# Optimization experiments

Hardware: AMD Instinct MI355X
Metric: run time of the kernel (lower is better)

## Reference

```python
import jax, jax.numpy as jnp
import numpy as np

N_NODES = 1048576
N_GRAPHS = 4096
NODES_PER_GRAPH = N_NODES // N_GRAPHS
N_EDGES = 8388608
F_IN = 16
HID = 32


def _glorot(k, shp):
    return jax.random.normal(k, shp, jnp.float32) * np.float32(np.sqrt(2.0 / (shp[-2] + shp[-1])))


def setup_inputs() -> dict:
    key = jax.random.key(0)
    ks = jax.random.split(key, 8)
    d = F_IN + HID  # DCRNN gate convs act on cat([X, H])
    return {
        "x": jax.random.normal(ks[0], (N_NODES, F_IN), jnp.float32),
        "edge_index": jax.random.randint(ks[1], (2, N_EDGES), 0, N_NODES),
        "edge_weight": jax.random.uniform(ks[2], (N_EDGES,), jnp.float32),
        "batch": jnp.repeat(jnp.arange(N_GRAPHS), NODES_PER_GRAPH),
        "W_z": _glorot(ks[3], (2, 1, d, HID)),
        "b_z": jnp.zeros((HID,), jnp.float32),
        "W_r": _glorot(ks[4], (2, 1, d, HID)),
        "b_r": jnp.zeros((HID,), jnp.float32),
        "W_h": _glorot(ks[5], (2, 1, d, HID)),
        "b_h": jnp.zeros((HID,), jnp.float32),
        "W_lin": _glorot(ks[6], (HID, 1)),
        "b_lin": jnp.zeros((1,), jnp.float32),
    }


def _dconv_k1(X, W, b):
    # torch_geometric_temporal DConv with K=1: the diffusion loop never runs,
    # so H = X @ W[0,0] + X @ W[1,0] + b (edge_index/edge_weight unused).
    return X @ (W[0, 0] + W[1, 0]) + b


def reference(x, edge_index, edge_weight, batch, W_z, b_z, W_r, b_r, W_h, b_h, W_lin, b_lin):
    del edge_index, edge_weight  # mathematically unused when K=1
    h0 = jnp.zeros((x.shape[0], HID), x.dtype)  # DCRNN hidden state default
    xh = jnp.concatenate([x, h0], axis=1)
    Z = jax.nn.sigmoid(_dconv_k1(xh, W_z, b_z))
    R = jax.nn.sigmoid(_dconv_k1(xh, W_r, b_r))
    xhr = jnp.concatenate([x, h0 * R], axis=1)
    H_tilde = jnp.tanh(_dconv_k1(xhr, W_h, b_h))
    H = Z * h0 + (1.0 - Z) * H_tilde  # (N, 32)
    h = jax.nn.relu(H)
    h = h @ W_lin + b_lin  # (N, 1)
    # global_mean_pool over per-node graph ids
    sums = jax.ops.segment_sum(h, batch, num_segments=N_GRAPHS)
    cnts = jax.ops.segment_sum(jnp.ones((h.shape[0], 1), h.dtype), batch, num_segments=N_GRAPHS)
    return sums / jnp.maximum(cnts, 1.0)  # (N_GRAPHS, 1)
```

## Files before the change

kernel.cpp:

```cpp
#include <hip/hip_runtime.h>

#define N_GRAPHS  4096
#define NPG       256
#define F_IN      16
#define HID       32
#define LOG2E     1.4426950408889634f

#define WS_FLOATS 609

typedef _Float16 half8  __attribute__((ext_vector_type(8)));
typedef float    f32x16 __attribute__((ext_vector_type(16)));

#if __has_builtin(__builtin_amdgcn_exp2f)
#define EXP2(x) __builtin_amdgcn_exp2f(x)
#else
#define EXP2(x) exp2f(x)
#endif

union FragU { uint4 u; half8 h; };

__device__ __forceinline__ uint4 make_frag32(int f, int l,
    const float* __restrict__ Wz, const float* __restrict__ Wh)
{
    const int col = l & 31, p = l >> 5;
    const float s = (f == 0) ? LOG2E : 2.0f * LOG2E;
    const float* W = (f == 0) ? Wz : Wh;
    FragU u;
#pragma unroll
    for (int j = 0; j < 8; ++j) {
        const int k = p * 8 + j;
        u.h[j] = (_Float16)((W[k * 32 + col] + W[1536 + k * 32 + col]) * s);
    }
    return u.u;
}

__global__ __launch_bounds__(256) void prep_kernel(
    const float* __restrict__ Wz, const float* __restrict__ bz,
    const float* __restrict__ Wh, const float* __restrict__ bh,
    const float* __restrict__ Wlin, const float* __restrict__ blin,
    float* __restrict__ w)
{
    const int t = threadIdx.x;
    if (t < 128) ((uint4*)w)[t] = make_frag32(t >> 6, t & 63, Wz, Wh);
    if (t < HID) {
        w[512 + t] = bz[t] * LOG2E;
        w[544 + t] = bh[t] * (2.0f * LOG2E);
        w[576 + t] = Wlin[t];
    }
    if (t == 0) w[608] = blin[0];
}

__device__ __forceinline__ float gate_term(float az, float ah, float wl, float osum)
{
    const float e1 = EXP2(az);
    const float e2 = EXP2(fminf(ah, 126.0f));
    const float r  = __builtin_amdgcn_rcpf((1.0f + e1) * (e2 + 1.0f));
    float v = (e2 - 1.0f) * r;
    v = v > 0.0f ? v : 0.0f;
    return fmaf(v, wl, osum);
}

__device__ __forceinline__ float tile32(float4 c0, float4 c1,
    half8 Bz, half8 Bh, float bzl, float bhl, float wll, float osum)
{
    const float xf[8] = { c0.x, c0.y, c0.z, c0.w, c1.x, c1.y, c1.z, c1.w };
    half8 Ah, Al;
#pragma unroll
    for (int j = 0; j < 8; ++j) {
        const _Float16 h = (_Float16)xf[j];
        Ah[j] = h;
        Al[j] = (_Float16)(xf[j] - (float)h);
    }
    f32x16 accZ, accH;
#pragma unroll
    for (int i = 0; i < 16; ++i) { accZ[i] = bzl; accH[i] = bhl; }
    accZ = __builtin_amdgcn_mfma_f32_32x32x16_f16(Ah, Bz, accZ, 0, 0, 0);
    accH = __builtin_amdgcn_mfma_f32_32x32x16_f16(Ah, Bh, accH, 0, 0, 0);
    accZ = __builtin_amdgcn_mfma_f32_32x32x16_f16(Al, Bz, accZ, 0, 0, 0);
    accH = __builtin_amdgcn_mfma_f32_32x32x16_f16(Al, Bh, accH, 0, 0, 0);
#pragma unroll
    for (int i = 0; i < 16; ++i)
        osum = gate_term(accZ[i], accH[i], wll, osum);
    return osum;
}

__device__ __forceinline__ void gcn_body(const float* __restrict__ x,
                                         const float* __restrict__ w,
                                         float* __restrict__ out, int g, int t)
{
    const int lane = t & 63, wv = t >> 6;
    const int col = lane & 31, p = lane >> 5;

    const uint4* bq = (const uint4*)w;
    FragU uz, uh;
    uz.u = bq[lane];
    uh.u = bq[64 + lane];

    const float bzl = w[512 + col];
    const float bhl = w[544 + col];
    const float wll = w[576 + col];

    const float* xw = x + ((size_t)g * NPG + wv * 64 + col) * F_IN + p * 8;
    const float4 a0 = *(const float4*)(xw);
    const float4 a1 = *(const float4*)(xw + 4);
    const float4 b0 = *(const float4*)(xw + 512);
    const float4 b1 = *(const float4*)(xw + 512 + 4);

    float osum = tile32(a0, a1, uz.h, uh.h, bzl, bhl, wll, 0.0f);
    osum       = tile32(b0, b1, uz.h, uh.h, bzl, bhl, wll, osum);

#pragma unroll
    for (int off = 32; off > 0; off >>= 1)
        osum += __shfl_down(osum, off, 64);
    __shared__ float part[4];
    if (lane == 0) part[wv] = osum;
    __syncthreads();
    if (t == 0)
        out[g] = (part[0] + part[1] + part[2] + part[3]) * (1.0f / (float)NPG)
               + w[608];
}

__global__ __launch_bounds__(256, 5) void gcn_main(
    const float* __restrict__ x, const float* __restrict__ w, float* __restrict__ out)
{
    gcn_body(x, w, out, blockIdx.x, threadIdx.x);
}

__global__ __launch_bounds__(256, 5) void gcn_main_lds(
    const float* __restrict__ x,
    const float* __restrict__ Wz, const float* __restrict__ bz,
    const float* __restrict__ Wh, const float* __restrict__ bh,
    const float* __restrict__ Wlin, const float* __restrict__ blin,
    float* __restrict__ out)
{
    __shared__ __attribute__((aligned(16))) float w[WS_FLOATS];
    const int t = threadIdx.x;
    if (t < 128) ((uint4*)w)[t] = make_frag32(t >> 6, t & 63, Wz, Wh);
    if (t < HID) {
        w[512 + t] = bz[t] * LOG2E;
        w[544 + t] = bh[t] * (2.0f * LOG2E);
        w[576 + t] = Wlin[t];
    }
    if (t == 0) w[608] = blin[0];
    __syncthreads();
    gcn_body(x, w, out, blockIdx.x, t);
}

extern "C" void kernel_launch(void* const* d_in, const int* in_sizes, int n_in,
                              void* d_out, int out_size, void* d_ws, size_t ws_size,
                              hipStream_t stream)
{
    const float* x    = (const float*)d_in[0];
    const float* Wz   = (const float*)d_in[4];
    const float* bz   = (const float*)d_in[5];
    const float* Wh   = (const float*)d_in[8];
    const float* bh   = (const float*)d_in[9];
    const float* Wlin = (const float*)d_in[10];
    const float* blin = (const float*)d_in[11];
    float* out = (float*)d_out;

    if (ws_size >= WS_FLOATS * sizeof(float)) {
        float* w = (float*)d_ws;
        prep_kernel<<<1, 256, 0, stream>>>(Wz, bz, Wh, bh, Wlin, blin, w);
        gcn_main<<<N_GRAPHS, NPG, 0, stream>>>(x, w, out);
    } else {
        gcn_main_lds<<<N_GRAPHS, NPG, 0, stream>>>(x, Wz, bz, Wh, bh, Wlin, blin, out);
    }
}
```

Baseline: 178.4 us.

## Assign one graph per wavefront with register-prefetched loop over node tiles

Each wavefront now processes a whole graph (8 tiles of 32 nodes) instead of four waves splitting one graph. The next tile's inputs are loaded before the current tile is computed, a software prefetch. This removes the LDS partial-sum exchange and __syncthreads, and cuts the grid to 1024 blocks. In exchange each wave does more serial work with higher register pressure (launch bounds lowered to 4 blocks per SM), and there are fewer waves in flight to hide memory latency.

```diff
diff --git a/kernel.cpp b/kernel.cpp
--- a/kernel.cpp
+++ b/kernel.cpp
@@ -84,11 +84,10 @@
     return osum;
 }
 
-__device__ __forceinline__ void gcn_body(const float* __restrict__ x,
+__device__ __forceinline__ void gcn_wave(const float* __restrict__ x,
                                          const float* __restrict__ w,
-                                         float* __restrict__ out, int g, int t)
+                                         float* __restrict__ out, int g, int lane)
 {
-    const int lane = t & 63, wv = t >> 6;
     const int col = lane & 31, p = lane >> 5;
 
     const uint4* bq = (const uint4*)w;
@@ -100,33 +99,36 @@
     const float bhl = w[544 + col];
     const float wll = w[576 + col];
 
-    const float* xw = x + ((size_t)g * NPG + wv * 64 + col) * F_IN + p * 8;
-    const float4 a0 = *(const float4*)(xw);
-    const float4 a1 = *(const float4*)(xw + 4);
-    const float4 b0 = *(const float4*)(xw + 512);
-    const float4 b1 = *(const float4*)(xw + 512 + 4);
+    const float* xw = x + ((size_t)g * NPG + col) * F_IN + p * 8;
+    float4 c0 = *(const float4*)(xw);
+    float4 c1 = *(const float4*)(xw + 4);
+    float osum = 0.0f;
 
-    float osum = tile32(a0, a1, uz.h, uh.h, bzl, bhl, wll, 0.0f);
-    osum       = tile32(b0, b1, uz.h, uh.h, bzl, bhl, wll, osum);
+#pragma unroll
+    for (int t = 0; t < 8; ++t) {
+        float4 n0 = c0, n1 = c1;
+        if (t < 7) {
+            n0 = *(const float4*)(xw + (t + 1) * 512);
+            n1 = *(const float4*)(xw + (t + 1) * 512 + 4);
+        }
+        osum = tile32(c0, c1, uz.h, uh.h, bzl, bhl, wll, osum);
+        c0 = n0; c1 = n1;
+    }
 
 #pragma unroll
     for (int off = 32; off > 0; off >>= 1)
         osum += __shfl_down(osum, off, 64);
-    __shared__ float part[4];
-    if (lane == 0) part[wv] = osum;
-    __syncthreads();
-    if (t == 0)
-        out[g] = (part[0] + part[1] + part[2] + part[3]) * (1.0f / (float)NPG)
-               + w[608];
+    if (lane == 0)
+        out[g] = osum * (1.0f / (float)NPG) + w[608];
 }
 
-__global__ __launch_bounds__(256, 5) void gcn_main(
+__global__ __launch_bounds__(256, 4) void gcn_main(
     const float* __restrict__ x, const float* __restrict__ w, float* __restrict__ out)
 {
-    gcn_body(x, w, out, blockIdx.x, threadIdx.x);
+    gcn_wave(x, w, out, blockIdx.x * 4 + (threadIdx.x >> 6), threadIdx.x & 63);
 }
 
-__global__ __launch_bounds__(256, 5) void gcn_main_lds(
+__global__ __launch_bounds__(256, 4) void gcn_main_lds(
     const float* __restrict__ x,
     const float* __restrict__ Wz, const float* __restrict__ bz,
     const float* __restrict__ Wh, const float* __restrict__ bh,
@@ -143,7 +145,7 @@
     }
     if (t == 0) w[608] = blin[0];
     __syncthreads();
-    gcn_body(x, w, out, blockIdx.x, t);
+    gcn_wave(x, w, out, blockIdx.x * 4 + (t >> 6), t & 63);
 }
 
 extern "C" void kernel_launch(void* const* d_in, const int* in_sizes, int n_in,
@@ -162,8 +164,8 @@
     if (ws_size >= WS_FLOATS * sizeof(float)) {
         float* w = (float*)d_ws;
         prep_kernel<<<1, 256, 0, stream>>>(Wz, bz, Wh, bh, Wlin, blin, w);
-        gcn_main<<<N_GRAPHS, NPG, 0, stream>>>(x, w, out);
+        gcn_main<<<N_GRAPHS / 4, 256, 0, stream>>>(x, w, out);
     } else {
-        gcn_main_lds<<<N_GRAPHS, NPG, 0, stream>>>(x, Wz, bz, Wh, bh, Wlin, blin, out);
+        gcn_main_lds<<<N_GRAPHS / 4, 256, 0, stream>>>(x, Wz, bz, Wh, bh, Wlin, blin, out);
     }
 }
```

Measured after the change: 173.5 us. 1.03x faster.
